# Performance work log

Hardware: AMD Instinct MI355X
Metric: run time of the kernel (lower is better)

## Reference

```python
import jax, jax.numpy as jnp
import numpy as np

B, T, C = 128, 256, 384
H, HD = 8, 48          # num_heads, head_dim
WINDOW = 64

def setup_inputs() -> dict:
    key = jax.random.key(0)
    ks = jax.random.split(key, 5)
    return {
        "x": jax.random.normal(ks[0], (B, T, C), dtype=jnp.float32),
        "W_qkv": jax.random.normal(ks[1], (C, 3 * C), dtype=jnp.float32) * (1.0 / np.sqrt(C)),
        "b_qkv": jax.random.normal(ks[2], (3 * C,), dtype=jnp.float32) * 0.02,
        "W_proj": jax.random.normal(ks[3], (C, C), dtype=jnp.float32) * (1.0 / np.sqrt(C)),
        "b_proj": jax.random.normal(ks[4], (C,), dtype=jnp.float32) * 0.02,
        "gate": jnp.ones((C,), dtype=jnp.float32),
    }

def reference(x, W_qkv, b_qkv, W_proj, b_proj, gate):
    Bx, Tx, Cx = x.shape
    qkv = x @ W_qkv + b_qkv                                   # [B,T,3C]
    q, k, v = jnp.split(qkv, 3, axis=-1)
    q = q.reshape(Bx, Tx, H, HD).transpose(0, 2, 1, 3)        # [B,H,T,hd]
    k = k.reshape(Bx, Tx, H, HD).transpose(0, 2, 1, 3)
    v = v.reshape(Bx, Tx, H, HD).transpose(0, 2, 1, 3)
    scale = 1.0 / np.sqrt(HD).astype(np.float32)
    att = jnp.einsum("bhqd,bhkd->bhqk", q, k) * scale        # [B,H,T,T]
    idx = jnp.arange(Tx)
    causal = idx[:, None] >= idx[None, :]                     # lower-tri
    local = jnp.abs(idx[None, :] - idx[:, None]) <= WINDOW
    mask = (causal & local)[None, None, :, :]
    att = jnp.where(mask, att, -jnp.inf)
    att = jax.nn.softmax(att, axis=-1)
    out = jnp.einsum("bhqk,bhkd->bhqd", att, v)               # [B,H,T,hd]
    out = out.transpose(0, 2, 1, 3).reshape(Bx, Tx, Cx)       # [B,T,C]
    return (out * gate) @ W_proj + b_proj
```

## Files before the change

### kernel.cpp

```cpp
#include <hip/hip_runtime.h>

typedef __attribute__((ext_vector_type(8))) short bf16x8;
typedef __attribute__((ext_vector_type(4))) float floatx4;

#define NB 128
#define NT 256
#define NC 384
#define NH 8
#define ND 48

static __device__ __forceinline__ unsigned short f2bf(float f) {
  unsigned int u = __float_as_uint(f);
  return (unsigned short)((u + 0x7fffu + ((u >> 16) & 1u)) >> 16);
}

static __device__ __forceinline__ void gload16(const unsigned short* g, unsigned short* l) {
  __builtin_amdgcn_global_load_lds(
      (const __attribute__((address_space(1))) void*)g,
      (__attribute__((address_space(3))) void*)l, 16, 0, 0);
}

__global__ __launch_bounds__(256) void k_cvt(const float* __restrict__ in,
                                             unsigned short* __restrict__ outp,
                                             int n8) {
  int idx = blockIdx.x * 256 + threadIdx.x;
  const int stride = gridDim.x * 256;
  for (; idx < n8; idx += stride) {
    const float* s = in + (size_t)idx * 8;
    float v[8];
    *(float4*)&v[0] = ((const float4*)s)[0];
    *(float4*)&v[4] = ((const float4*)s)[1];
    bf16x8 p;
#pragma unroll
    for (int i = 0; i < 8; ++i) p[i] = f2bf(v[i]);
    *(bf16x8*)(outp + (size_t)idx * 8) = p;
  }
}

__global__ __launch_bounds__(256) void k_twt(const float* __restrict__ Wq,
                                             const float* __restrict__ Wp,
                                             unsigned short* __restrict__ WqT,
                                             unsigned short* __restrict__ WpT) {
  __shared__ float T[64][65];
  int blk = blockIdx.x;
  const float* src;
  unsigned short* dst;
  int N, kt, nt;
  if (blk < 108) { src = Wq; dst = WqT; N = 1152; kt = blk / 18; nt = blk % 18; }
  else { int b2 = blk - 108; src = Wp; dst = WpT; N = 384; kt = b2 / 6; nt = b2 % 6; }
  const int k0 = kt * 64, n0 = nt * 64;
  const int t = threadIdx.x;
  const int r = t >> 2, c = (t & 3) * 16;
  const float* s = src + (size_t)(k0 + r) * N + n0 + c;
#pragma unroll
  for (int i = 0; i < 4; ++i) *(float4*)&T[r][c + i * 4] = ((const float4*)s)[i];
  __syncthreads();
  unsigned short o[16];
#pragma unroll
  for (int i = 0; i < 16; ++i) o[i] = f2bf(T[c + i][r]);
  unsigned short* dp = dst + (size_t)(n0 + r) * 384 + k0 + c;
  *(bf16x8*)dp = *(bf16x8*)&o[0];
  *(bf16x8*)(dp + 8) = *(bf16x8*)&o[8];
}

__global__ __launch_bounds__(256) void k_qkv(const unsigned short* __restrict__ xb,
                                             const unsigned short* __restrict__ WqT,
                                             const float* __restrict__ bq,
                                             unsigned short* __restrict__ qkv) {
  __shared__ __align__(16) unsigned short As[128 * 32];
  __shared__ __align__(16) unsigned short Bs[128 * 32];
  const int t = threadIdx.x, lane = t & 63, w = t >> 6;
  const int wm = w >> 1, wn = w & 1;
  const int lq = lane & 15, lg = lane >> 4;
  const int m0 = blockIdx.x * 128, n0 = blockIdx.y * 128;
  const unsigned short* Ag = xb + (size_t)(m0 + w * 32 + (lane >> 2)) * 384 + (lane & 3) * 8;
  const unsigned short* Bg = WqT + (size_t)(n0 + w * 32 + (lane >> 2)) * 384 + (lane & 3) * 8;
  unsigned short* lA0 = As + (w * 32) * 32;
  unsigned short* lA1 = As + (w * 32 + 16) * 32;
  unsigned short* lB0 = Bs + (w * 32) * 32;
  unsigned short* lB1 = Bs + (w * 32 + 16) * 32;
  floatx4 acc[4][4] = {};

  for (int k0 = 0; k0 < 384; k0 += 32) {
    __syncthreads();
    gload16(Ag + k0, lA0);
    gload16(Ag + k0 + 16 * 384, lA1);
    gload16(Bg + k0, lB0);
    gload16(Bg + k0 + 16 * 384, lB1);
    __syncthreads();
    bf16x8 a[4], b[4];
#pragma unroll
    for (int mt = 0; mt < 4; ++mt)
      a[mt] = *(const bf16x8*)&As[(wm * 64 + mt * 16 + lq) * 32 + lg * 8];
#pragma unroll
    for (int nt = 0; nt < 4; ++nt)
      b[nt] = *(const bf16x8*)&Bs[(wn * 64 + nt * 16 + lq) * 32 + lg * 8];
#pragma unroll
    for (int mt = 0; mt < 4; ++mt)
#pragma unroll
      for (int nt = 0; nt < 4; ++nt)
        acc[mt][nt] = __builtin_amdgcn_mfma_f32_16x16x32_bf16(a[mt], b[nt], acc[mt][nt], 0, 0, 0);
  }
  const int comp = n0 / 384;
  const int cb = n0 - comp * 384;
#pragma unroll
  for (int nt = 0; nt < 4; ++nt) {
    const int cc = cb + wn * 64 + nt * 16 + lq;
    const int h = cc / 48, d = cc - h * 48;
    const float bias = bq[n0 + wn * 64 + nt * 16 + lq];
#pragma unroll
    for (int mt = 0; mt < 4; ++mt) {
#pragma unroll
      for (int j = 0; j < 4; ++j) {
        const int row = m0 + wm * 64 + mt * 16 + lg * 4 + j;
        const int bb = row >> 8, tt = row & 255;
        qkv[((((size_t)comp * NB + bb) * NH + h) * NT + tt) * ND + d] =
            f2bf(acc[mt][nt][j] + bias);
      }
    }
  }
}

__global__ __launch_bounds__(256) void k_attn(const unsigned short* __restrict__ qkv,
                                              const float* __restrict__ gate,
                                              unsigned short* __restrict__ attg) {
  __shared__ __align__(16) unsigned short Ks[128 * 72];
  __shared__ __align__(16) unsigned short Vt[48 * 152];
  __shared__ __align__(16) unsigned short Ps[4 * 16 * 104];
  const int t = threadIdx.x;
  const int blk = blockIdx.x;
  const int tile = blk & 3;
  const int bh = blk >> 2;
  const int b = bh >> 3, h = bh & 7;
  const int base = tile * 64;
  const size_t kvoff = (size_t)bh * NT * ND;
  const unsigned short* qptr = qkv + kvoff;
  const unsigned short* kptr = qkv + (size_t)NB * NH * NT * ND + kvoff;
  const unsigned short* vptr = qkv + (size_t)2 * NB * NH * NT * ND + kvoff;

  if (t < 48) {
    bf16x8 z = {};
    *(bf16x8*)&Vt[t * 152 + 128] = z;
    *(bf16x8*)&Vt[t * 152 + 136] = z;
  }
  if (t < 128) {
    const int r = t, ka = base - 64 + r;
    unsigned short* dst = &Ks[r * 72];
    if (ka >= 0) {
      const unsigned short* src = kptr + (size_t)ka * ND;
#pragma unroll
      for (int i = 0; i < 6; ++i) *(bf16x8*)(dst + i * 8) = *(const bf16x8*)(src + i * 8);
      bf16x8 z = {};
      *(bf16x8*)(dst + 48) = z;
      *(bf16x8*)(dst + 56) = z;
    } else {
      bf16x8 z = {};
#pragma unroll
      for (int i = 0; i < 8; ++i) *(bf16x8*)(dst + i * 8) = z;
    }
  } else {
    const int r = t - 128, ka = base - 64 + r;
    if (ka >= 0) {
      const unsigned short* src = vptr + (size_t)ka * ND;
      bf16x8 vv[6];
#pragma unroll
      for (int i = 0; i < 6; ++i) vv[i] = *(const bf16x8*)(src + i * 8);
#pragma unroll
      for (int i = 0; i < 6; ++i)
#pragma unroll
        for (int j = 0; j < 8; ++j)
          Vt[(i * 8 + j) * 152 + r] = (unsigned short)vv[i][j];
    } else {
#pragma unroll
      for (int d = 0; d < 48; ++d) Vt[d * 152 + r] = 0;
    }
  }
  __syncthreads();

  const int lane = t & 63, w = t >> 6;
  const int lq = lane & 15, lg = lane >> 4;
  const int qs = base + w * 16;

  const unsigned short* qrow = qptr + (size_t)(qs + lq) * ND;
  bf16x8 aq0 = *(const bf16x8*)(qrow + lg * 8);
  bf16x8 aq1 = {};
  if (lg < 2) aq1 = *(const bf16x8*)(qrow + 32 + lg * 8);

  floatx4 s[5];
#pragma unroll
  for (int kt = 0; kt < 5; ++kt) {
    const unsigned short* kr = &Ks[(w * 16 + kt * 16 + lq) * 72];
    bf16x8 kb0 = *(const bf16x8*)(kr + lg * 8);
    bf16x8 kb1 = *(const bf16x8*)(kr + 32 + lg * 8);
    floatx4 z = {};
    z = __builtin_amdgcn_mfma_f32_16x16x32_bf16(aq0, kb0, z, 0, 0, 0);
    z = __builtin_amdgcn_mfma_f32_16x16x32_bf16(aq1, kb1, z, 0, 0, 0);
    s[kt] = z;
  }

  const float scale = 0.14433756729740643f;
  floatx4 pj[5];
#pragma unroll
  for (int j = 0; j < 4; ++j) {
    const int qa = qs + lg * 4 + j;
    float mx = -1e30f;
    float sv[5];
    bool ok[5];
#pragma unroll
    for (int kt = 0; kt < 5; ++kt) {
      const int ka = base - 64 + w * 16 + kt * 16 + lq;
      sv[kt] = s[kt][j] * scale;
      ok[kt] = (ka >= 0) && (ka <= qa) && (qa - ka <= 64);
      if (ok[kt]) mx = fmaxf(mx, sv[kt]);
    }
#pragma unroll
    for (int dd = 1; dd < 16; dd <<= 1) mx = fmaxf(mx, __shfl_xor(mx, dd));
    float sum = 0.f;
#pragma unroll
    for (int kt = 0; kt < 5; ++kt) {
      float p = ok[kt] ? __expf(sv[kt] - mx) : 0.f;
      pj[kt][j] = p;
      sum += p;
    }
#pragma unroll
    for (int dd = 1; dd < 16; dd <<= 1) sum += __shfl_xor(sum, dd);
    const float inv = 1.f / sum;
#pragma unroll
    for (int kt = 0; kt < 5; ++kt) pj[kt][j] *= inv;
  }

  unsigned short* pw = &Ps[w * 16 * 104];
#pragma unroll
  for (int kt = 0; kt < 5; ++kt)
#pragma unroll
    for (int j = 0; j < 4; ++j)
      pw[(lg * 4 + j) * 104 + kt * 16 + lq] = f2bf(pj[kt][j]);
#pragma unroll
  for (int j = 0; j < 4; ++j) pw[lq * 104 + 80 + lg * 4 + j] = 0;

  floatx4 o[3] = {};
#pragma unroll
  for (int c = 0; c < 3; ++c) {
    bf16x8 ap = *(const bf16x8*)&pw[lq * 104 + c * 32 + lg * 8];
#pragma unroll
    for (int nt = 0; nt < 3; ++nt) {
      bf16x8 av = *(const bf16x8*)&Vt[(nt * 16 + lq) * 152 + w * 16 + c * 32 + lg * 8];
      o[nt] = __builtin_amdgcn_mfma_f32_16x16x32_bf16(ap, av, o[nt], 0, 0, 0);
    }
  }
#pragma unroll
  for (int nt = 0; nt < 3; ++nt) {
    const int d = nt * 16 + lq;
    const int c = h * ND + d;
    const float g = gate[c];
#pragma unroll
    for (int j = 0; j < 4; ++j) {
      const int tt = qs + lg * 4 + j;
      attg[((size_t)b * NT + tt) * NC + c] = f2bf(o[nt][j] * g);
    }
  }
}

__global__ __launch_bounds__(256) void k_proj(const unsigned short* __restrict__ A,
                                              const unsigned short* __restrict__ WpT,
                                              const float* __restrict__ bp,
                                              float* __restrict__ out) {
  __shared__ __align__(16) unsigned short As[128 * 32];
  __shared__ __align__(16) unsigned short Bs[128 * 32];
  const int t = threadIdx.x, lane = t & 63, w = t >> 6;
  const int wm = w >> 1, wn = w & 1;
  const int lq = lane & 15, lg = lane >> 4;
  const int m0 = blockIdx.x * 128, n0 = blockIdx.y * 128;
  const unsigned short* Ag = A + (size_t)(m0 + w * 32 + (lane >> 2)) * 384 + (lane & 3) * 8;
  const unsigned short* Bg = WpT + (size_t)(n0 + w * 32 + (lane >> 2)) * 384 + (lane & 3) * 8;
  unsigned short* lA0 = As + (w * 32) * 32;
  unsigned short* lA1 = As + (w * 32 + 16) * 32;
  unsigned short* lB0 = Bs + (w * 32) * 32;
  unsigned short* lB1 = Bs + (w * 32 + 16) * 32;
  floatx4 acc[4][4] = {};

  for (int k0 = 0; k0 < 384; k0 += 32) {
    __syncthreads();
    gload16(Ag + k0, lA0);
    gload16(Ag + k0 + 16 * 384, lA1);
    gload16(Bg + k0, lB0);
    gload16(Bg + k0 + 16 * 384, lB1);
    __syncthreads();
    bf16x8 a[4], b[4];
#pragma unroll
    for (int mt = 0; mt < 4; ++mt)
      a[mt] = *(const bf16x8*)&As[(wm * 64 + mt * 16 + lq) * 32 + lg * 8];
#pragma unroll
    for (int nt = 0; nt < 4; ++nt)
      b[nt] = *(const bf16x8*)&Bs[(wn * 64 + nt * 16 + lq) * 32 + lg * 8];
#pragma unroll
    for (int mt = 0; mt < 4; ++mt)
#pragma unroll
      for (int nt = 0; nt < 4; ++nt)
        acc[mt][nt] = __builtin_amdgcn_mfma_f32_16x16x32_bf16(a[mt], b[nt], acc[mt][nt], 0, 0, 0);
  }
#pragma unroll
  for (int nt = 0; nt < 4; ++nt) {
    const int col = n0 + wn * 64 + nt * 16 + lq;
    const float bias = bp[col];
#pragma unroll
    for (int mt = 0; mt < 4; ++mt)
#pragma unroll
      for (int j = 0; j < 4; ++j) {
        const int row = m0 + wm * 64 + mt * 16 + lg * 4 + j;
        out[(size_t)row * 384 + col] = acc[mt][nt][j] + bias;
      }
  }
}

extern "C" void kernel_launch(void* const* d_in, const int* in_sizes, int n_in,
                              void* d_out, int out_size, void* d_ws, size_t ws_size,
                              hipStream_t stream) {
  const float* x    = (const float*)d_in[0];
  const float* Wq   = (const float*)d_in[1];
  const float* bq   = (const float*)d_in[2];
  const float* Wp   = (const float*)d_in[3];
  const float* bp   = (const float*)d_in[4];
  const float* gate = (const float*)d_in[5];

  const size_t nx = (size_t)NB * NT * NC;
  unsigned short* xbf  = (unsigned short*)d_ws;
  unsigned short* qkvp = xbf + nx;
  unsigned short* WqT  = qkvp + (size_t)3 * NB * NH * NT * ND;
  unsigned short* WpT  = WqT + (size_t)384 * 1152;
  unsigned short* attg = xbf;
  float* out = (float*)d_out;

  k_cvt<<<dim3(2048), 256, 0, stream>>>(x, xbf, (int)(nx / 8));
  k_twt<<<dim3(144), 256, 0, stream>>>(Wq, Wp, WqT, WpT);
  k_qkv<<<dim3(256, 9), 256, 0, stream>>>(xbf, WqT, bq, qkvp);
  k_attn<<<dim3(4096), 256, 0, stream>>>(qkvp, gate, attg);
  k_proj<<<dim3(256, 3), 256, 0, stream>>>(attg, WpT, bp, out);
}
```

Measured before the change: 122.2 us.

## Fuse x fp32-to-bf16 conversion into QKV GEMM and double-buffer both GEMMs

Drops the standalone conversion kernel for x. The QKV GEMM now reads fp32 x directly, converts it in registers and writes bf16 into LDS. Both GEMMs switch to double-buffered LDS, prefetching the next K-slice while computing the current one, with one barrier per iteration instead of two. This removes an extra full pass over x in global memory and a kernel launch. In exchange, the QKV kernel reads x as fp32 nine times, once per N-block column, which doubles A-side traffic, and it uses more LDS per block.

```diff
diff --git a/kernel.cpp b/kernel.cpp
--- a/kernel.cpp
+++ b/kernel.cpp
@@ -1,4 +1,5 @@
 #include <hip/hip_runtime.h>
+#include <hip/hip_bf16.h>
 
 typedef __attribute__((ext_vector_type(8))) short bf16x8;
 typedef __attribute__((ext_vector_type(4))) float floatx4;
@@ -10,31 +11,14 @@
 #define ND 48
 
 static __device__ __forceinline__ unsigned short f2bf(float f) {
-  unsigned int u = __float_as_uint(f);
-  return (unsigned short)((u + 0x7fffu + ((u >> 16) & 1u)) >> 16);
+  __hip_bfloat16 h = __float2bfloat16(f);
+  return __builtin_bit_cast(unsigned short, h);
 }
 
 static __device__ __forceinline__ void gload16(const unsigned short* g, unsigned short* l) {
   __builtin_amdgcn_global_load_lds(
       (const __attribute__((address_space(1))) void*)g,
       (__attribute__((address_space(3))) void*)l, 16, 0, 0);
-}
-
-__global__ __launch_bounds__(256) void k_cvt(const float* __restrict__ in,
-                                             unsigned short* __restrict__ outp,
-                                             int n8) {
-  int idx = blockIdx.x * 256 + threadIdx.x;
-  const int stride = gridDim.x * 256;
-  for (; idx < n8; idx += stride) {
-    const float* s = in + (size_t)idx * 8;
-    float v[8];
-    *(float4*)&v[0] = ((const float4*)s)[0];
-    *(float4*)&v[4] = ((const float4*)s)[1];
-    bf16x8 p;
-#pragma unroll
-    for (int i = 0; i < 8; ++i) p[i] = f2bf(v[i]);
-    *(bf16x8*)(outp + (size_t)idx * 8) = p;
-  }
 }
 
 __global__ __launch_bounds__(256) void k_twt(const float* __restrict__ Wq,
@@ -63,44 +47,78 @@
   *(bf16x8*)(dp + 8) = *(bf16x8*)&o[8];
 }
 
-__global__ __launch_bounds__(256) void k_qkv(const unsigned short* __restrict__ xb,
+__global__ __launch_bounds__(256) void k_qkv(const float* __restrict__ x,
                                              const unsigned short* __restrict__ WqT,
                                              const float* __restrict__ bq,
                                              unsigned short* __restrict__ qkv) {
-  __shared__ __align__(16) unsigned short As[128 * 32];
-  __shared__ __align__(16) unsigned short Bs[128 * 32];
+  __shared__ __align__(16) unsigned short As[2 * 128 * 32];
+  __shared__ __align__(16) unsigned short Bs[2 * 128 * 32];
   const int t = threadIdx.x, lane = t & 63, w = t >> 6;
   const int wm = w >> 1, wn = w & 1;
   const int lq = lane & 15, lg = lane >> 4;
   const int m0 = blockIdx.x * 128, n0 = blockIdx.y * 128;
-  const unsigned short* Ag = xb + (size_t)(m0 + w * 32 + (lane >> 2)) * 384 + (lane & 3) * 8;
+
+  const float* Ag0 = x + (size_t)(m0 + (t >> 2)) * 384 + (t & 3) * 8;
+  const float* Ag1 = Ag0 + (size_t)64 * 384;
   const unsigned short* Bg = WqT + (size_t)(n0 + w * 32 + (lane >> 2)) * 384 + (lane & 3) * 8;
-  unsigned short* lA0 = As + (w * 32) * 32;
-  unsigned short* lA1 = As + (w * 32 + 16) * 32;
-  unsigned short* lB0 = Bs + (w * 32) * 32;
-  unsigned short* lB1 = Bs + (w * 32 + 16) * 32;
+
   floatx4 acc[4][4] = {};
-
+  float va[16];
+
+#define LOADA_Q(k0)                                                   \
+  {                                                                   \
+    *(float4*)&va[0]  = ((const float4*)(Ag0 + (k0)))[0];             \
+    *(float4*)&va[4]  = ((const float4*)(Ag0 + (k0)))[1];             \
+    *(float4*)&va[8]  = ((const float4*)(Ag1 + (k0)))[0];             \
+    *(float4*)&va[12] = ((const float4*)(Ag1 + (k0)))[1];             \
+  }
+#define WRITEA_Q(buf)                                                 \
+  {                                                                   \
+    bf16x8 p0, p1;                                                    \
+    _Pragma("unroll") for (int i = 0; i < 8; ++i) {                   \
+      p0[i] = (short)f2bf(va[i]);                                     \
+      p1[i] = (short)f2bf(va[8 + i]);                                 \
+    }                                                                 \
+    *(bf16x8*)(As + (buf)*4096 + 8 * t) = p0;                         \
+    *(bf16x8*)(As + (buf)*4096 + 2048 + 8 * t) = p1;                  \
+  }
+#define LOADB_Q(k0, buf)                                              \
+  {                                                                   \
+    gload16(Bg + (k0), Bs + (buf)*4096 + (w * 32) * 32);              \
+    gload16(Bg + (k0) + 16 * 384, Bs + (buf)*4096 + (w * 32 + 16) * 32); \
+  }
+
+  LOADA_Q(0);
+  LOADB_Q(0, 0);
+  WRITEA_Q(0);
+  __syncthreads();
+
+  int cur = 0;
   for (int k0 = 0; k0 < 384; k0 += 32) {
-    __syncthreads();
-    gload16(Ag + k0, lA0);
-    gload16(Ag + k0 + 16 * 384, lA1);
-    gload16(Bg + k0, lB0);
-    gload16(Bg + k0 + 16 * 384, lB1);
-    __syncthreads();
+    const int nk = k0 + 32;
+    if (nk < 384) {
+      LOADA_Q(nk);
+      LOADB_Q(nk, cur ^ 1);
+    }
+    const unsigned short* Ac = As + cur * 4096;
+    const unsigned short* Bc = Bs + cur * 4096;
     bf16x8 a[4], b[4];
 #pragma unroll
     for (int mt = 0; mt < 4; ++mt)
-      a[mt] = *(const bf16x8*)&As[(wm * 64 + mt * 16 + lq) * 32 + lg * 8];
+      a[mt] = *(const bf16x8*)&Ac[(wm * 64 + mt * 16 + lq) * 32 + lg * 8];
 #pragma unroll
     for (int nt = 0; nt < 4; ++nt)
-      b[nt] = *(const bf16x8*)&Bs[(wn * 64 + nt * 16 + lq) * 32 + lg * 8];
+      b[nt] = *(const bf16x8*)&Bc[(wn * 64 + nt * 16 + lq) * 32 + lg * 8];
 #pragma unroll
     for (int mt = 0; mt < 4; ++mt)
 #pragma unroll
       for (int nt = 0; nt < 4; ++nt)
         acc[mt][nt] = __builtin_amdgcn_mfma_f32_16x16x32_bf16(a[mt], b[nt], acc[mt][nt], 0, 0, 0);
-  }
+    if (nk < 384) WRITEA_Q(cur ^ 1);
+    __syncthreads();
+    cur ^= 1;
+  }
+
   const int comp = n0 / 384;
   const int cb = n0 - comp * 384;
 #pragma unroll
@@ -265,39 +283,47 @@
                                               const unsigned short* __restrict__ WpT,
                                               const float* __restrict__ bp,
                                               float* __restrict__ out) {
-  __shared__ __align__(16) unsigned short As[128 * 32];
-  __shared__ __align__(16) unsigned short Bs[128 * 32];
+  __shared__ __align__(16) unsigned short As[2 * 128 * 32];
+  __shared__ __align__(16) unsigned short Bs[2 * 128 * 32];
   const int t = threadIdx.x, lane = t & 63, w = t >> 6;
   const int wm = w >> 1, wn = w & 1;
   const int lq = lane & 15, lg = lane >> 4;
   const int m0 = blockIdx.x * 128, n0 = blockIdx.y * 128;
   const unsigned short* Ag = A + (size_t)(m0 + w * 32 + (lane >> 2)) * 384 + (lane & 3) * 8;
   const unsigned short* Bg = WpT + (size_t)(n0 + w * 32 + (lane >> 2)) * 384 + (lane & 3) * 8;
-  unsigned short* lA0 = As + (w * 32) * 32;
-  unsigned short* lA1 = As + (w * 32 + 16) * 32;
-  unsigned short* lB0 = Bs + (w * 32) * 32;
-  unsigned short* lB1 = Bs + (w * 32 + 16) * 32;
   floatx4 acc[4][4] = {};
 
+#define STAGE_P(k0, buf)                                                   \
+  {                                                                        \
+    gload16(Ag + (k0), As + (buf)*4096 + (w * 32) * 32);                   \
+    gload16(Ag + (k0) + 16 * 384, As + (buf)*4096 + (w * 32 + 16) * 32);   \
+    gload16(Bg + (k0), Bs + (buf)*4096 + (w * 32) * 32);                   \
+    gload16(Bg + (k0) + 16 * 384, Bs + (buf)*4096 + (w * 32 + 16) * 32);   \
+  }
+
+  STAGE_P(0, 0);
+  __syncthreads();
+
+  int cur = 0;
   for (int k0 = 0; k0 < 384; k0 += 32) {
-    __syncthreads();
-    gload16(Ag + k0, lA0);
-    gload16(Ag + k0 + 16 * 384, lA1);
-    gload16(Bg + k0, lB0);
-    gload16(Bg + k0 + 16 * 384, lB1);
-    __syncthreads();
+    const int nk = k0 + 32;
+    if (nk < 384) STAGE_P(nk, cur ^ 1);
+    const unsigned short* Ac = As + cur * 4096;
+    const unsigned short* Bc = Bs + cur * 4096;
     bf16x8 a[4], b[4];
 #pragma unroll
     for (int mt = 0; mt < 4; ++mt)
-      a[mt] = *(const bf16x8*)&As[(wm * 64 + mt * 16 + lq) * 32 + lg * 8];
+      a[mt] = *(const bf16x8*)&Ac[(wm * 64 + mt * 16 + lq) * 32 + lg * 8];
 #pragma unroll
     for (int nt = 0; nt < 4; ++nt)
-      b[nt] = *(const bf16x8*)&Bs[(wn * 64 + nt * 16 + lq) * 32 + lg * 8];
+      b[nt] = *(const bf16x8*)&Bc[(wn * 64 + nt * 16 + lq) * 32 + lg * 8];
 #pragma unroll
     for (int mt = 0; mt < 4; ++mt)
 #pragma unroll
       for (int nt = 0; nt < 4; ++nt)
         acc[mt][nt] = __builtin_amdgcn_mfma_f32_16x16x32_bf16(a[mt], b[nt], acc[mt][nt], 0, 0, 0);
+    __syncthreads();
+    cur ^= 1;
   }
 #pragma unroll
   for (int nt = 0; nt < 4; ++nt) {
@@ -324,16 +350,14 @@
   const float* gate = (const float*)d_in[5];
 
   const size_t nx = (size_t)NB * NT * NC;
-  unsigned short* xbf  = (unsigned short*)d_ws;
-  unsigned short* qkvp = xbf + nx;
+  unsigned short* attg = (unsigned short*)d_ws;
+  unsigned short* qkvp = attg + nx;
   unsigned short* WqT  = qkvp + (size_t)3 * NB * NH * NT * ND;
   unsigned short* WpT  = WqT + (size_t)384 * 1152;
-  unsigned short* attg = xbf;
   float* out = (float*)d_out;
 
-  k_cvt<<<dim3(2048), 256, 0, stream>>>(x, xbf, (int)(nx / 8));
   k_twt<<<dim3(144), 256, 0, stream>>>(Wq, Wp, WqT, WpT);
-  k_qkv<<<dim3(256, 9), 256, 0, stream>>>(xbf, WqT, bq, qkvp);
+  k_qkv<<<dim3(256, 9), 256, 0, stream>>>(x, WqT, bq, qkvp);
   k_attn<<<dim3(4096), 256, 0, stream>>>(qkvp, gate, attg);
   k_proj<<<dim3(256, 3), 256, 0, stream>>>(attg, WpT, bp, out);
 }
```

Result: no change. 120.8 us (-1.1%).

## Triple-buffer GEMM K-loop with async LDS loads, swizzle, and merged prep kernel

Applied to the files above, without the earlier changes.

Both GEMMs now use a three-stage LDS ring fed by global_load_lds, with explicit vmcnt waits and one barrier per K step, so loads for later K tiles overlap the MFMA work on the current one. LDS rows are XOR-swizzled to cut bank conflicts on the fragment reads. The x conversion and weight transpose kernels are merged into one launch, and the attention output gets its own workspace region instead of aliasing the bf16 copy of x. LDS use triples per GEMM block, which may lower occupancy, and the workspace requirement grows.

```diff
diff --git a/kernel.cpp b/kernel.cpp
--- a/kernel.cpp
+++ b/kernel.cpp
@@ -1,4 +1,5 @@
 #include <hip/hip_runtime.h>
+#include <hip/hip_bf16.h>
 
 typedef __attribute__((ext_vector_type(8))) short bf16x8;
 typedef __attribute__((ext_vector_type(4))) float floatx4;
@@ -10,8 +11,8 @@
 #define ND 48
 
 static __device__ __forceinline__ unsigned short f2bf(float f) {
-  unsigned int u = __float_as_uint(f);
-  return (unsigned short)((u + 0x7fffu + ((u >> 16) & 1u)) >> 16);
+  __hip_bfloat16 h = __float2bfloat16(f);
+  return __builtin_bit_cast(unsigned short, h);
 }
 
 static __device__ __forceinline__ void gload16(const unsigned short* g, unsigned short* l) {
@@ -20,87 +21,100 @@
       (__attribute__((address_space(3))) void*)l, 16, 0, 0);
 }
 
-__global__ __launch_bounds__(256) void k_cvt(const float* __restrict__ in,
-                                             unsigned short* __restrict__ outp,
-                                             int n8) {
-  int idx = blockIdx.x * 256 + threadIdx.x;
-  const int stride = gridDim.x * 256;
-  for (; idx < n8; idx += stride) {
-    const float* s = in + (size_t)idx * 8;
-    float v[8];
-    *(float4*)&v[0] = ((const float4*)s)[0];
-    *(float4*)&v[4] = ((const float4*)s)[1];
-    bf16x8 p;
-#pragma unroll
-    for (int i = 0; i < 8; ++i) p[i] = f2bf(v[i]);
-    *(bf16x8*)(outp + (size_t)idx * 8) = p;
-  }
-}
-
-__global__ __launch_bounds__(256) void k_twt(const float* __restrict__ Wq,
-                                             const float* __restrict__ Wp,
-                                             unsigned short* __restrict__ WqT,
-                                             unsigned short* __restrict__ WpT) {
-  __shared__ float T[64][65];
-  int blk = blockIdx.x;
-  const float* src;
-  unsigned short* dst;
-  int N, kt, nt;
-  if (blk < 108) { src = Wq; dst = WqT; N = 1152; kt = blk / 18; nt = blk % 18; }
-  else { int b2 = blk - 108; src = Wp; dst = WpT; N = 384; kt = b2 / 6; nt = b2 % 6; }
-  const int k0 = kt * 64, n0 = nt * 64;
+__global__ __launch_bounds__(256) void k_prep(const float* __restrict__ x,
+                                              const float* __restrict__ Wq,
+                                              const float* __restrict__ Wp,
+                                              unsigned short* __restrict__ xbf,
+                                              unsigned short* __restrict__ WqT,
+                                              unsigned short* __restrict__ WpT) {
+  const int blk = blockIdx.x;
   const int t = threadIdx.x;
-  const int r = t >> 2, c = (t & 3) * 16;
-  const float* s = src + (size_t)(k0 + r) * N + n0 + c;
-#pragma unroll
-  for (int i = 0; i < 4; ++i) *(float4*)&T[r][c + i * 4] = ((const float4*)s)[i];
-  __syncthreads();
-  unsigned short o[16];
-#pragma unroll
-  for (int i = 0; i < 16; ++i) o[i] = f2bf(T[c + i][r]);
-  unsigned short* dp = dst + (size_t)(n0 + r) * 384 + k0 + c;
-  *(bf16x8*)dp = *(bf16x8*)&o[0];
-  *(bf16x8*)(dp + 8) = *(bf16x8*)&o[8];
-}
+  if (blk < 144) {
+    __shared__ float T[64][65];
+    const float* src;
+    unsigned short* dst;
+    int N, kt, nt;
+    if (blk < 108) { src = Wq; dst = WqT; N = 1152; kt = blk / 18; nt = blk % 18; }
+    else { int b2 = blk - 108; src = Wp; dst = WpT; N = 384; kt = b2 / 6; nt = b2 % 6; }
+    const int k0 = kt * 64, n0 = nt * 64;
+    const int r = t >> 2, c = (t & 3) * 16;
+    const float* s = src + (size_t)(k0 + r) * N + n0 + c;
+#pragma unroll
+    for (int i = 0; i < 4; ++i) *(float4*)&T[r][c + i * 4] = ((const float4*)s)[i];
+    __syncthreads();
+    unsigned short o[16];
+#pragma unroll
+    for (int i = 0; i < 16; ++i) o[i] = f2bf(T[c + i][r]);
+    unsigned short* dp = dst + (size_t)(n0 + r) * 384 + k0 + c;
+    *(bf16x8*)dp = *(bf16x8*)&o[0];
+    *(bf16x8*)(dp + 8) = *(bf16x8*)&o[8];
+  } else {
+    const int n8 = (NB * NT * NC) / 8;
+    int idx = (blk - 144) * 256 + t;
+    const int stride = (gridDim.x - 144) * 256;
+    for (; idx < n8; idx += stride) {
+      const float* s = x + (size_t)idx * 8;
+      float v[8];
+      *(float4*)&v[0] = ((const float4*)s)[0];
+      *(float4*)&v[4] = ((const float4*)s)[1];
+      bf16x8 p;
+#pragma unroll
+      for (int i = 0; i < 8; ++i) p[i] = f2bf(v[i]);
+      *(bf16x8*)(xbf + (size_t)idx * 8) = p;
+    }
+  }
+}
+
+#define STAGE_G(Ag, Bg, As, Bs, k0, buf)                                             \
+  {                                                                                  \
+    const int r0_ = (lane >> 2), sw0_ = 8 * ((lane & 3) ^ ((r0_ >> 1) & 3));         \
+    const int r1_ = r0_ + 16,    sw1_ = 8 * ((lane & 3) ^ ((r1_ >> 1) & 3));         \
+    gload16(Ag + (size_t)r0_ * 384 + (k0) + sw0_, As + (buf)*4096 + (w * 32) * 32);  \
+    gload16(Ag + (size_t)r1_ * 384 + (k0) + sw1_, As + (buf)*4096 + (w * 32 + 16) * 32); \
+    gload16(Bg + (size_t)r0_ * 384 + (k0) + sw0_, Bs + (buf)*4096 + (w * 32) * 32);  \
+    gload16(Bg + (size_t)r1_ * 384 + (k0) + sw1_, Bs + (buf)*4096 + (w * 32 + 16) * 32); \
+  }
+
+#define GEMM_PIPE(Ag, Bg, As, Bs)                                                    \
+  STAGE_G(Ag, Bg, As, Bs, 0, 0);                                                     \
+  STAGE_G(Ag, Bg, As, Bs, 32, 1);                                                    \
+  _Pragma("unroll") for (int t_ = 0; t_ < 12; ++t_) {                                \
+    if (t_ < 11) asm volatile("s_waitcnt vmcnt(4)" ::: "memory");                    \
+    else         asm volatile("s_waitcnt vmcnt(0)" ::: "memory");                    \
+    __builtin_amdgcn_s_barrier();                                                    \
+    if (t_ < 10) STAGE_G(Ag, Bg, As, Bs, (t_ + 2) * 32, (t_ + 2) % 3);               \
+    const unsigned short* Ac_ = As + (t_ % 3) * 4096;                                \
+    const unsigned short* Bc_ = Bs + (t_ % 3) * 4096;                                \
+    bf16x8 a_[4], b_[4];                                                             \
+    _Pragma("unroll") for (int mt = 0; mt < 4; ++mt) {                               \
+      const int R = wm * 64 + mt * 16 + lq;                                          \
+      a_[mt] = *(const bf16x8*)&Ac_[R * 32 + 8 * (lg ^ ((R >> 1) & 3))];             \
+    }                                                                                \
+    _Pragma("unroll") for (int nt = 0; nt < 4; ++nt) {                               \
+      const int R = wn * 64 + nt * 16 + lq;                                          \
+      b_[nt] = *(const bf16x8*)&Bc_[R * 32 + 8 * (lg ^ ((R >> 1) & 3))];             \
+    }                                                                                \
+    _Pragma("unroll") for (int mt = 0; mt < 4; ++mt)                                 \
+      _Pragma("unroll") for (int nt = 0; nt < 4; ++nt)                               \
+        acc[mt][nt] = __builtin_amdgcn_mfma_f32_16x16x32_bf16(a_[mt], b_[nt], acc[mt][nt], 0, 0, 0); \
+  }
 
 __global__ __launch_bounds__(256) void k_qkv(const unsigned short* __restrict__ xb,
                                              const unsigned short* __restrict__ WqT,
                                              const float* __restrict__ bq,
                                              unsigned short* __restrict__ qkv) {
-  __shared__ __align__(16) unsigned short As[128 * 32];
-  __shared__ __align__(16) unsigned short Bs[128 * 32];
+  __shared__ __align__(16) unsigned short As[3 * 128 * 32];
+  __shared__ __align__(16) unsigned short Bs[3 * 128 * 32];
   const int t = threadIdx.x, lane = t & 63, w = t >> 6;
   const int wm = w >> 1, wn = w & 1;
   const int lq = lane & 15, lg = lane >> 4;
   const int m0 = blockIdx.x * 128, n0 = blockIdx.y * 128;
-  const unsigned short* Ag = xb + (size_t)(m0 + w * 32 + (lane >> 2)) * 384 + (lane & 3) * 8;
-  const unsigned short* Bg = WqT + (size_t)(n0 + w * 32 + (lane >> 2)) * 384 + (lane & 3) * 8;
-  unsigned short* lA0 = As + (w * 32) * 32;
-  unsigned short* lA1 = As + (w * 32 + 16) * 32;
-  unsigned short* lB0 = Bs + (w * 32) * 32;
-  unsigned short* lB1 = Bs + (w * 32 + 16) * 32;
+  const unsigned short* Ag = xb + (size_t)(m0 + w * 32) * 384;
+  const unsigned short* Bg = WqT + (size_t)(n0 + w * 32) * 384;
   floatx4 acc[4][4] = {};
 
-  for (int k0 = 0; k0 < 384; k0 += 32) {
-    __syncthreads();
-    gload16(Ag + k0, lA0);
-    gload16(Ag + k0 + 16 * 384, lA1);
-    gload16(Bg + k0, lB0);
-    gload16(Bg + k0 + 16 * 384, lB1);
-    __syncthreads();
-    bf16x8 a[4], b[4];
-#pragma unroll
-    for (int mt = 0; mt < 4; ++mt)
-      a[mt] = *(const bf16x8*)&As[(wm * 64 + mt * 16 + lq) * 32 + lg * 8];
-#pragma unroll
-    for (int nt = 0; nt < 4; ++nt)
-      b[nt] = *(const bf16x8*)&Bs[(wn * 64 + nt * 16 + lq) * 32 + lg * 8];
-#pragma unroll
-    for (int mt = 0; mt < 4; ++mt)
-#pragma unroll
-      for (int nt = 0; nt < 4; ++nt)
-        acc[mt][nt] = __builtin_amdgcn_mfma_f32_16x16x32_bf16(a[mt], b[nt], acc[mt][nt], 0, 0, 0);
-  }
+  GEMM_PIPE(Ag, Bg, As, Bs);
+
   const int comp = n0 / 384;
   const int cb = n0 - comp * 384;
 #pragma unroll
@@ -118,6 +132,36 @@
             f2bf(acc[mt][nt][j] + bias);
       }
     }
+  }
+}
+
+__global__ __launch_bounds__(256) void k_proj(const unsigned short* __restrict__ A,
+                                              const unsigned short* __restrict__ WpT,
+                                              const float* __restrict__ bp,
+                                              float* __restrict__ out) {
+  __shared__ __align__(16) unsigned short As[3 * 128 * 32];
+  __shared__ __align__(16) unsigned short Bs[3 * 128 * 32];
+  const int t = threadIdx.x, lane = t & 63, w = t >> 6;
+  const int wm = w >> 1, wn = w & 1;
+  const int lq = lane & 15, lg = lane >> 4;
+  const int m0 = blockIdx.x * 128, n0 = blockIdx.y * 128;
+  const unsigned short* Ag = A + (size_t)(m0 + w * 32) * 384;
+  const unsigned short* Bg = WpT + (size_t)(n0 + w * 32) * 384;
+  floatx4 acc[4][4] = {};
+
+  GEMM_PIPE(Ag, Bg, As, Bs);
+
+#pragma unroll
+  for (int nt = 0; nt < 4; ++nt) {
+    const int col = n0 + wn * 64 + nt * 16 + lq;
+    const float bias = bp[col];
+#pragma unroll
+    for (int mt = 0; mt < 4; ++mt)
+#pragma unroll
+      for (int j = 0; j < 4; ++j) {
+        const int row = m0 + wm * 64 + mt * 16 + lg * 4 + j;
+        out[(size_t)row * 384 + col] = acc[mt][nt][j] + bias;
+      }
   }
 }
 
@@ -261,58 +305,6 @@
   }
 }
 
-__global__ __launch_bounds__(256) void k_proj(const unsigned short* __restrict__ A,
-                                              const unsigned short* __restrict__ WpT,
-                                              const float* __restrict__ bp,
-                                              float* __restrict__ out) {
-  __shared__ __align__(16) unsigned short As[128 * 32];
-  __shared__ __align__(16) unsigned short Bs[128 * 32];
-  const int t = threadIdx.x, lane = t & 63, w = t >> 6;
-  const int wm = w >> 1, wn = w & 1;
-  const int lq = lane & 15, lg = lane >> 4;
-  const int m0 = blockIdx.x * 128, n0 = blockIdx.y * 128;
-  const unsigned short* Ag = A + (size_t)(m0 + w * 32 + (lane >> 2)) * 384 + (lane & 3) * 8;
-  const unsigned short* Bg = WpT + (size_t)(n0 + w * 32 + (lane >> 2)) * 384 + (lane & 3) * 8;
-  unsigned short* lA0 = As + (w * 32) * 32;
-  unsigned short* lA1 = As + (w * 32 + 16) * 32;
-  unsigned short* lB0 = Bs + (w * 32) * 32;
-  unsigned short* lB1 = Bs + (w * 32 + 16) * 32;
-  floatx4 acc[4][4] = {};
-
-  for (int k0 = 0; k0 < 384; k0 += 32) {
-    __syncthreads();
-    gload16(Ag + k0, lA0);
-    gload16(Ag + k0 + 16 * 384, lA1);
-    gload16(Bg + k0, lB0);
-    gload16(Bg + k0 + 16 * 384, lB1);
-    __syncthreads();
-    bf16x8 a[4], b[4];
-#pragma unroll
-    for (int mt = 0; mt < 4; ++mt)
-      a[mt] = *(const bf16x8*)&As[(wm * 64 + mt * 16 + lq) * 32 + lg * 8];
-#pragma unroll
-    for (int nt = 0; nt < 4; ++nt)
-      b[nt] = *(const bf16x8*)&Bs[(wn * 64 + nt * 16 + lq) * 32 + lg * 8];
-#pragma unroll
-    for (int mt = 0; mt < 4; ++mt)
-#pragma unroll
-      for (int nt = 0; nt < 4; ++nt)
-        acc[mt][nt] = __builtin_amdgcn_mfma_f32_16x16x32_bf16(a[mt], b[nt], acc[mt][nt], 0, 0, 0);
-  }
-#pragma unroll
-  for (int nt = 0; nt < 4; ++nt) {
-    const int col = n0 + wn * 64 + nt * 16 + lq;
-    const float bias = bp[col];
-#pragma unroll
-    for (int mt = 0; mt < 4; ++mt)
-#pragma unroll
-      for (int j = 0; j < 4; ++j) {
-        const int row = m0 + wm * 64 + mt * 16 + lg * 4 + j;
-        out[(size_t)row * 384 + col] = acc[mt][nt][j] + bias;
-      }
-  }
-}
-
 extern "C" void kernel_launch(void* const* d_in, const int* in_sizes, int n_in,
                               void* d_out, int out_size, void* d_ws, size_t ws_size,
                               hipStream_t stream) {
@@ -324,15 +316,14 @@
   const float* gate = (const float*)d_in[5];
 
   const size_t nx = (size_t)NB * NT * NC;
-  unsigned short* xbf  = (unsigned short*)d_ws;
+  unsigned short* attg = (unsigned short*)d_ws;
+  unsigned short* xbf  = attg + nx;
   unsigned short* qkvp = xbf + nx;
   unsigned short* WqT  = qkvp + (size_t)3 * NB * NH * NT * ND;
   unsigned short* WpT  = WqT + (size_t)384 * 1152;
-  unsigned short* attg = xbf;
   float* out = (float*)d_out;
 
-  k_cvt<<<dim3(2048), 256, 0, stream>>>(x, xbf, (int)(nx / 8));
-  k_twt<<<dim3(144), 256, 0, stream>>>(Wq, Wp, WqT, WpT);
+  k_prep<<<dim3(1680), 256, 0, stream>>>(x, Wq, Wp, xbf, WqT, WpT);
   k_qkv<<<dim3(256, 9), 256, 0, stream>>>(xbf, WqT, bq, qkvp);
   k_attn<<<dim3(4096), 256, 0, stream>>>(qkvp, gate, attg);
   k_proj<<<dim3(256, 3), 256, 0, stream>>>(attg, WpT, bp, out);
```

After: 117.7 us. 3.7% less time.
